# Kernel optimization log

Hardware: AMD Instinct MI355X
Metric: run time of the kernel (lower is better)

The kernel has to match this reference:

```python
import jax, jax.numpy as jnp
from jax import lax
import numpy as np

B, T, F, H, O = 4096, 2048, 8, 32, 8


def setup_inputs() -> dict:
    key = jax.random.key(0)
    k = jax.random.split(key, 7)
    s = 1.0 / np.sqrt(H).astype(np.float32)  # torch RNN/Linear init bound
    x = jax.random.normal(k[0], (B, T, F), dtype=jnp.float32)
    W_ih = jax.random.uniform(k[1], (H, F), minval=-s, maxval=s, dtype=jnp.float32)
    W_hh = jax.random.uniform(k[2], (H, H), minval=-s, maxval=s, dtype=jnp.float32)
    b_ih = jax.random.uniform(k[3], (H,), minval=-s, maxval=s, dtype=jnp.float32)
    b_hh = jax.random.uniform(k[4], (H,), minval=-s, maxval=s, dtype=jnp.float32)
    W_out = jax.random.uniform(k[5], (O, H), minval=-s, maxval=s, dtype=jnp.float32)
    b_out = jax.random.uniform(k[6], (O,), minval=-s, maxval=s, dtype=jnp.float32)
    return {"x": x, "W_ih": W_ih, "W_hh": W_hh, "b_ih": b_ih, "b_hh": b_hh,
            "W_out": W_out, "b_out": b_out}


def reference(x, W_ih, W_hh, b_ih, b_hh, W_out, b_out):
    # Precompute input projection for all timesteps: [B, T, H]
    xp = jnp.einsum('btf,hf->bth', x, W_ih) + b_ih + b_hh
    h0 = jnp.zeros((x.shape[0], W_hh.shape[0]), dtype=x.dtype)

    def step(h, xt):  # xt: [B, H]
        h = jnp.tanh(xt + h @ W_hh.T)
        return h, None

    h_final, _ = lax.scan(step, h0, jnp.swapaxes(xp, 0, 1))  # scan over T
    # torch returns out(h) with h of shape [num_layers=1, B, H]
    y = h_final @ W_out.T + b_out  # [B, O]
    return y[None]  # [1, B, O]
```

## Files before the change

### kernel.cpp

```cpp
#include <hip/hip_runtime.h>


typedef float v2f __attribute__((ext_vector_type(2)));
typedef _Float16 h2v __attribute__((ext_vector_type(2)));

static constexpr int T_STEPS = 2048;
static constexpr int FDIM    = 8;
static constexpr int HDIM    = 32;
static constexpr int ODIM    = 8;
static constexpr int ROWS_PER_BLOCK = 8;
static constexpr int GROUP   = 4;
static constexpr int NGROUP  = T_STEPS / GROUP;
static constexpr int LSTR    = 40;

__device__ __forceinline__ float fdot2(h2v a, h2v b, float c) {
    return __builtin_amdgcn_fdot2(a, b, c, false);
}
__device__ __forceinline__ h2v bch(unsigned u) {
    return __builtin_bit_cast(h2v, u);
}

__global__ __launch_bounds__(256, 2) void rnn_scan_kernel(
    const float* __restrict__ x,
    const float* __restrict__ W_ih,
    const float* __restrict__ W_hh,
    const float* __restrict__ b_ih,
    const float* __restrict__ b_hh,
    const float* __restrict__ W_out,
    const float* __restrict__ b_out,
    float* __restrict__ out)
{
    const float K = 2.8853900817779268f;
    const int tid  = threadIdx.x;
    const int lane = tid & 63;
    const int wave = tid >> 6;
    const int g    = lane & 15;
    const int c    = (lane >> 4) & 1;
    const int sub  = lane >> 5;
    const int r    = wave * 2 + sub;
    const long long b = (long long)blockIdx.x * ROWS_PER_BLOCK + r;
    const int d0 = 2 * g, d1 = 2 * g + 1;

    __shared__ _Float16 hsh[ROWS_PER_BLOCK][LSTR];

    h2v wA[8], wB[8];
    const float* whr0 = W_hh + d0 * HDIM + 16 * c;
    const float* whr1 = W_hh + d1 * HDIM + 16 * c;
#pragma unroll
    for (int j = 0; j < 8; ++j) {
        h2v wa; wa[0] = (_Float16)(whr0[2 * j] * K); wa[1] = (_Float16)(whr0[2 * j + 1] * K);
        wA[j] = wa;
        h2v wb; wb[0] = (_Float16)(whr1[2 * j] * K); wb[1] = (_Float16)(whr1[2 * j + 1] * K);
        wB[j] = wb;
    }
    v2f wiv[4];
#pragma unroll
    for (int f = 0; f < 4; ++f) {
        v2f w; w[0] = W_ih[d0 * FDIM + 4 * c + f] * K;
               w[1] = W_ih[d1 * FDIM + 4 * c + f] * K;
        wiv[f] = w;
    }
    v2f bias2;
    bias2[0] = c ? 0.0f : (b_ih[d0] + b_hh[d0]) * K;
    bias2[1] = c ? 0.0f : (b_ih[d1] + b_hh[d1]) * K;

    hsh[r][2 * g + c] = (_Float16)0.0f;

    const float4* xq = reinterpret_cast<const float4*>(x + (size_t)b * T_STEPS * FDIM);
    const uint4* hq = reinterpret_cast<const uint4*>(
        reinterpret_cast<const char*>(&hsh[r][0]) + 32 * c);
    _Float16* hw = &hsh[r][2 * g + c];

#define LOADG(buf, gi)                                                         \
    {                                                                          \
        const int base = (gi) * (2 * GROUP) + c;                               \
        _Pragma("unroll")                                                      \
        for (int k = 0; k < GROUP; ++k) buf[k] = xq[base + 2 * k];             \
    }                                                                          \
    asm volatile("" ::: "memory");

#define STEP(xr)                                                               \
    {                                                                          \
        uint4 u0 = hq[0], u1 = hq[1];                                          \
        float c00 = 0.0f, c01 = 0.0f, c10 = 0.0f, c11 = 0.0f;                  \
        c00 = fdot2(wA[0], bch(u0.x), c00);  c10 = fdot2(wB[0], bch(u0.x), c10); \
        c01 = fdot2(wA[4], bch(u1.x), c01);  c11 = fdot2(wB[4], bch(u1.x), c11); \
        c00 = fdot2(wA[1], bch(u0.y), c00);  c10 = fdot2(wB[1], bch(u0.y), c10); \
        c01 = fdot2(wA[5], bch(u1.y), c01);  c11 = fdot2(wB[5], bch(u1.y), c11); \
        c00 = fdot2(wA[2], bch(u0.z), c00);  c10 = fdot2(wB[2], bch(u0.z), c10); \
        c01 = fdot2(wA[6], bch(u1.z), c01);  c11 = fdot2(wB[6], bch(u1.z), c11); \
        c00 = fdot2(wA[3], bch(u0.w), c00);  c10 = fdot2(wB[3], bch(u0.w), c10); \
        c01 = fdot2(wA[7], bch(u1.w), c01);  c11 = fdot2(wB[7], bch(u1.w), c11); \
        v2f a = bias2;                                                         \
        v2f t;                                                                 \
        t[0] = xr.x; t[1] = xr.x;  a = __builtin_elementwise_fma(wiv[0], t, a); \
        t[0] = xr.y; t[1] = xr.y;  a = __builtin_elementwise_fma(wiv[1], t, a); \
        t[0] = xr.z; t[1] = xr.z;  a = __builtin_elementwise_fma(wiv[2], t, a); \
        t[0] = xr.w; t[1] = xr.w;  a = __builtin_elementwise_fma(wiv[3], t, a); \
        v2f dotv; dotv[0] = c00 + c01; dotv[1] = c10 + c11;                    \
        v2f s2 = a + dotv;                                                     \
        float o0 = __int_as_float(__builtin_amdgcn_ds_swizzle(                 \
                       __float_as_int(s2[0]), 0x401f));                        \
        float o1 = __int_as_float(__builtin_amdgcn_ds_swizzle(                 \
                       __float_as_int(s2[1]), 0x401f));                        \
        float s = c ? (s2[1] + o1) : (s2[0] + o0);                             \
        float e = __builtin_amdgcn_exp2f(s);                                   \
        float rc = __builtin_amdgcn_rcpf(e + 1.0f);                            \
        *hw = (_Float16)fmaf(-2.0f, rc, 1.0f);                                 \
    }

#define STEPS(buf) STEP(buf[0]) STEP(buf[1]) STEP(buf[2]) STEP(buf[3])

    float4 bufA[GROUP], bufB[GROUP];
    LOADG(bufA, 0)

    for (int gi = 0; gi < NGROUP; gi += 2) {
        LOADG(bufB, gi + 1)
        STEPS(bufA)
        {
            const int gn = (gi + 2 < NGROUP) ? (gi + 2) : (NGROUP - 1);
            LOADG(bufA, gn)
        }
        STEPS(bufB)
    }
#undef STEPS
#undef STEP
#undef LOADG

    __syncthreads();
    if (tid < ROWS_PER_BLOCK * ODIM) {
        const int rr = tid >> 3;
        const int o  = tid & 7;
        float acc = b_out[o];
#pragma unroll
        for (int j = 0; j < HDIM; ++j)
            acc = fmaf((float)hsh[rr][j], W_out[o * HDIM + j], acc);
        out[((long long)blockIdx.x * ROWS_PER_BLOCK + rr) * ODIM + o] = acc;
    }
}

extern "C" void kernel_launch(void* const* d_in, const int* in_sizes, int n_in,
                              void* d_out, int out_size, void* d_ws, size_t ws_size,
                              hipStream_t stream) {
    const float* x     = (const float*)d_in[0];
    const float* W_ih  = (const float*)d_in[1];
    const float* W_hh  = (const float*)d_in[2];
    const float* b_ih  = (const float*)d_in[3];
    const float* b_hh  = (const float*)d_in[4];
    const float* W_out = (const float*)d_in[5];
    const float* b_out = (const float*)d_in[6];

    const int B = in_sizes[0] / (T_STEPS * FDIM);
    const int grid = B / ROWS_PER_BLOCK;

    rnn_scan_kernel<<<grid, 256, 0, stream>>>(
        x, W_ih, W_hh, b_ih, b_hh, W_out, b_out, (float*)d_out);
}
```

Measured before the change: 643.1 us.

## Use one wave per row with 4-lane split and DPP quad reduction

Remaps the thread layout so each wave handles one batch row, with 16 lane groups of 4 lanes each computing two hidden units over an 8-wide slice of the hidden vector. The cross-lane reduction uses two DPP quad-permute adds instead of a ds_swizzle, and each step now needs only 8 fdot2 per lane plus a single uint4 LDS read. Input is loaded as float2 slices with a larger prefetch group, rows per block drop to 4, and launch bounds allow 4 blocks per CU. The aim is a shorter per-step dependent chain on the serial recurrence, paid for with an extra reduction stage and more lanes doing redundant tanh work.

```diff
diff --git a/kernel.cpp b/kernel.cpp
--- a/kernel.cpp
+++ b/kernel.cpp
@@ -1,17 +1,15 @@
 #include <hip/hip_runtime.h>
 
 
-typedef float v2f __attribute__((ext_vector_type(2)));
 typedef _Float16 h2v __attribute__((ext_vector_type(2)));
 
 static constexpr int T_STEPS = 2048;
 static constexpr int FDIM    = 8;
 static constexpr int HDIM    = 32;
 static constexpr int ODIM    = 8;
-static constexpr int ROWS_PER_BLOCK = 8;
-static constexpr int GROUP   = 4;
+static constexpr int ROWS_PER_BLOCK = 4;
+static constexpr int GROUP   = 8;
 static constexpr int NGROUP  = T_STEPS / GROUP;
-static constexpr int LSTR    = 40;
 
 __device__ __forceinline__ float fdot2(h2v a, h2v b, float c) {
     return __builtin_amdgcn_fdot2(a, b, c, false);
@@ -20,7 +18,11 @@
     return __builtin_bit_cast(h2v, u);
 }
 
-__global__ __launch_bounds__(256, 2) void rnn_scan_kernel(
+#define QADD(v, ctrl)                                                          \
+    ((v) + __int_as_float(__builtin_amdgcn_mov_dpp(                            \
+               __float_as_int(v), (ctrl), 0xF, 0xF, true)))
+
+__global__ __launch_bounds__(256, 4) void rnn_scan_kernel(
     const float* __restrict__ x,
     const float* __restrict__ W_ih,
     const float* __restrict__ W_hh,
@@ -34,93 +36,77 @@
     const int tid  = threadIdx.x;
     const int lane = tid & 63;
     const int wave = tid >> 6;
-    const int g    = lane & 15;
-    const int c    = (lane >> 4) & 1;
-    const int sub  = lane >> 5;
-    const int r    = wave * 2 + sub;
-    const long long b = (long long)blockIdx.x * ROWS_PER_BLOCK + r;
+    const int g    = lane >> 2;
+    const int c    = lane & 3;
+    const long long b = (long long)blockIdx.x * ROWS_PER_BLOCK + wave;
     const int d0 = 2 * g, d1 = 2 * g + 1;
 
-    __shared__ _Float16 hsh[ROWS_PER_BLOCK][LSTR];
+    __shared__ _Float16 hsh[ROWS_PER_BLOCK][HDIM];
 
-    h2v wA[8], wB[8];
-    const float* whr0 = W_hh + d0 * HDIM + 16 * c;
-    const float* whr1 = W_hh + d1 * HDIM + 16 * c;
+    h2v w0[4], w1[4];
+    const float* whr0 = W_hh + d0 * HDIM + 8 * c;
+    const float* whr1 = W_hh + d1 * HDIM + 8 * c;
 #pragma unroll
-    for (int j = 0; j < 8; ++j) {
-        h2v wa; wa[0] = (_Float16)(whr0[2 * j] * K); wa[1] = (_Float16)(whr0[2 * j + 1] * K);
-        wA[j] = wa;
-        h2v wb; wb[0] = (_Float16)(whr1[2 * j] * K); wb[1] = (_Float16)(whr1[2 * j + 1] * K);
-        wB[j] = wb;
+    for (int j = 0; j < 4; ++j) {
+        h2v a; a[0] = (_Float16)(whr0[2 * j] * K); a[1] = (_Float16)(whr0[2 * j + 1] * K);
+        w0[j] = a;
+        h2v e; e[0] = (_Float16)(whr1[2 * j] * K); e[1] = (_Float16)(whr1[2 * j + 1] * K);
+        w1[j] = e;
     }
-    v2f wiv[4];
-#pragma unroll
-    for (int f = 0; f < 4; ++f) {
-        v2f w; w[0] = W_ih[d0 * FDIM + 4 * c + f] * K;
-               w[1] = W_ih[d1 * FDIM + 4 * c + f] * K;
-        wiv[f] = w;
-    }
-    v2f bias2;
-    bias2[0] = c ? 0.0f : (b_ih[d0] + b_hh[d0]) * K;
-    bias2[1] = c ? 0.0f : (b_ih[d1] + b_hh[d1]) * K;
+    const float wx00 = W_ih[d0 * FDIM + 2 * c]     * K;
+    const float wx01 = W_ih[d0 * FDIM + 2 * c + 1] * K;
+    const float wx10 = W_ih[d1 * FDIM + 2 * c]     * K;
+    const float wx11 = W_ih[d1 * FDIM + 2 * c + 1] * K;
+    const float bias0 = (b_ih[d0] + b_hh[d0]) * K * 0.25f;
+    const float bias1 = (b_ih[d1] + b_hh[d1]) * K * 0.25f;
 
-    hsh[r][2 * g + c] = (_Float16)0.0f;
+    hsh[wave][d0 + (c & 1)] = (_Float16)0.0f;
 
-    const float4* xq = reinterpret_cast<const float4*>(x + (size_t)b * T_STEPS * FDIM);
-    const uint4* hq = reinterpret_cast<const uint4*>(
-        reinterpret_cast<const char*>(&hsh[r][0]) + 32 * c);
-    _Float16* hw = &hsh[r][2 * g + c];
+    const uint4* hq = reinterpret_cast<const uint4*>(&hsh[wave][0]) + c;
+    _Float16* hw = &hsh[wave][d0 + (c & 1)];
+    const float2* xv = reinterpret_cast<const float2*>(x + (size_t)b * T_STEPS * FDIM);
 
 #define LOADG(buf, gi)                                                         \
     {                                                                          \
-        const int base = (gi) * (2 * GROUP) + c;                               \
+        const int base = (gi) * (GROUP * 4) + c;                               \
         _Pragma("unroll")                                                      \
-        for (int k = 0; k < GROUP; ++k) buf[k] = xq[base + 2 * k];             \
+        for (int k = 0; k < GROUP; ++k) buf[k] = xv[base + 4 * k];             \
     }                                                                          \
     asm volatile("" ::: "memory");
 
 #define STEP(xr)                                                               \
     {                                                                          \
-        uint4 u0 = hq[0], u1 = hq[1];                                          \
-        float c00 = 0.0f, c01 = 0.0f, c10 = 0.0f, c11 = 0.0f;                  \
-        c00 = fdot2(wA[0], bch(u0.x), c00);  c10 = fdot2(wB[0], bch(u0.x), c10); \
-        c01 = fdot2(wA[4], bch(u1.x), c01);  c11 = fdot2(wB[4], bch(u1.x), c11); \
-        c00 = fdot2(wA[1], bch(u0.y), c00);  c10 = fdot2(wB[1], bch(u0.y), c10); \
-        c01 = fdot2(wA[5], bch(u1.y), c01);  c11 = fdot2(wB[5], bch(u1.y), c11); \
-        c00 = fdot2(wA[2], bch(u0.z), c00);  c10 = fdot2(wB[2], bch(u0.z), c10); \
-        c01 = fdot2(wA[6], bch(u1.z), c01);  c11 = fdot2(wB[6], bch(u1.z), c11); \
-        c00 = fdot2(wA[3], bch(u0.w), c00);  c10 = fdot2(wB[3], bch(u0.w), c10); \
-        c01 = fdot2(wA[7], bch(u1.w), c01);  c11 = fdot2(wB[7], bch(u1.w), c11); \
-        v2f a = bias2;                                                         \
-        v2f t;                                                                 \
-        t[0] = xr.x; t[1] = xr.x;  a = __builtin_elementwise_fma(wiv[0], t, a); \
-        t[0] = xr.y; t[1] = xr.y;  a = __builtin_elementwise_fma(wiv[1], t, a); \
-        t[0] = xr.z; t[1] = xr.z;  a = __builtin_elementwise_fma(wiv[2], t, a); \
-        t[0] = xr.w; t[1] = xr.w;  a = __builtin_elementwise_fma(wiv[3], t, a); \
-        v2f dotv; dotv[0] = c00 + c01; dotv[1] = c10 + c11;                    \
-        v2f s2 = a + dotv;                                                     \
-        float o0 = __int_as_float(__builtin_amdgcn_ds_swizzle(                 \
-                       __float_as_int(s2[0]), 0x401f));                        \
-        float o1 = __int_as_float(__builtin_amdgcn_ds_swizzle(                 \
-                       __float_as_int(s2[1]), 0x401f));                        \
-        float s = c ? (s2[1] + o1) : (s2[0] + o0);                             \
+        float a0 = bias0, a1 = bias1;                                          \
+            \
+        a0 = fmaf(wx00, xr.x, a0);  a1 = fmaf(wx10, xr.x, a1);                 \
+        a0 = fmaf(wx01, xr.y, a0);  a1 = fmaf(wx11, xr.y, a1);                 \
+        uint4 u = hq[0];                                                       \
+        a0 = fdot2(w0[0], bch(u.x), a0);  a1 = fdot2(w1[0], bch(u.x), a1);     \
+        a0 = fdot2(w0[1], bch(u.y), a0);  a1 = fdot2(w1[1], bch(u.y), a1);     \
+        a0 = fdot2(w0[2], bch(u.z), a0);  a1 = fdot2(w1[2], bch(u.z), a1);     \
+        a0 = fdot2(w0[3], bch(u.w), a0);  a1 = fdot2(w1[3], bch(u.w), a1);     \
+              \
+        a0 = QADD(a0, 0xB1);  a1 = QADD(a1, 0xB1);                             \
+        a0 = QADD(a0, 0x4E);  a1 = QADD(a1, 0x4E);                             \
+        float s = (c & 1) ? a1 : a0;                                           \
         float e = __builtin_amdgcn_exp2f(s);                                   \
         float rc = __builtin_amdgcn_rcpf(e + 1.0f);                            \
         *hw = (_Float16)fmaf(-2.0f, rc, 1.0f);                                 \
     }
 
-#define STEPS(buf) STEP(buf[0]) STEP(buf[1]) STEP(buf[2]) STEP(buf[3])
+#define STEPS(buf)                                                             \
+    STEP(buf[0]) STEP(buf[1]) STEP(buf[2]) STEP(buf[3])                        \
+    STEP(buf[4]) STEP(buf[5]) STEP(buf[6]) STEP(buf[7])
 
-    float4 bufA[GROUP], bufB[GROUP];
+    float2 bufA[GROUP], bufB[GROUP];
     LOADG(bufA, 0)
 
     for (int gi = 0; gi < NGROUP; gi += 2) {
-        LOADG(bufB, gi + 1)
+        const int g1 = (gi + 1 < NGROUP) ? (gi + 1) : gi;
+        LOADG(bufB, g1)
         STEPS(bufA)
-        {
-            const int gn = (gi + 2 < NGROUP) ? (gi + 2) : (NGROUP - 1);
-            LOADG(bufA, gn)
-        }
+        const int g2 = (gi + 2 < NGROUP) ? (gi + 2) : gi;
+        LOADG(bufA, g2)
         STEPS(bufB)
     }
 #undef STEPS
```

After: 697.9 us. 1.09x slower.
